# Performance work log

Hardware: AMD Instinct MI355X
Metric: run time of the kernel (lower is better)

Reference implementation:

```python
import jax, jax.numpy as jnp
import numpy as np

DECAY = 0.99
EPS = 1e-5  # Laplace smoothing eps in cluster-size balancing


def _quantize(z_flat, embedding, cluster_size, emb_avg, n_codes):
    # z_flat: [N, D]; embedding: [K, D]
    d = (jnp.sum(z_flat * z_flat, axis=1, keepdims=True)
         + jnp.sum(embedding * embedding, axis=1)
         - 2.0 * (z_flat @ embedding.T))                      # [N, K]
    idx = jnp.argmin(d, axis=1)                               # [N]
    # EMA update (training path). segment_sum == one-hot matmul scatter-add.
    counts = jax.ops.segment_sum(jnp.ones(z_flat.shape[0], z_flat.dtype), idx,
                                 num_segments=n_codes)        # [K]
    new_cs = cluster_size * DECAY + (1.0 - DECAY) * counts
    dw = jax.ops.segment_sum(z_flat, idx, num_segments=n_codes)  # [K, D]
    new_avg = emb_avg * DECAY + (1.0 - DECAY) * dw
    n = new_cs.sum()
    bal = (new_cs + EPS) / (n + n_codes * EPS) * n
    # torch assigns via .data (no autograd) -> stop_gradient for faithfulness
    new_emb = jax.lax.stop_gradient(new_avg / bal[:, None])
    z_q = jnp.take(new_emb, idx, axis=0)  # == one_hot(idx) @ new_emb
    return idx, z_q


def _l2norm(x):
    # F.normalize(x, dim=-1) with eps=1e-12
    return x / jnp.maximum(jnp.linalg.norm(x, axis=-1, keepdims=True), 1e-12)


def reference(z, structure_embedding, style_embedding,
              structure_cluster_size, style_cluster_size,
              structure_embedding_avg, style_embedding_avg):
    b, c, h, w, d = z.shape
    zp = jnp.transpose(z, (0, 2, 3, 4, 1))      # b h w d c
    z_flat = zp.reshape(-1, c)                  # [N, D]
    s_idx, s_q = _quantize(z_flat, structure_embedding, structure_cluster_size,
                           structure_embedding_avg, structure_embedding.shape[0])
    y_idx, y_q = _quantize(z_flat, style_embedding, style_cluster_size,
                           style_embedding_avg, style_embedding.shape[0])

    def back(q):  # [N, C] -> b c h w d
        return jnp.transpose(q.reshape(b, h, w, d, c), (0, 4, 1, 2, 3))

    s_enc = back(s_q)
    y_enc = back(y_q)
    # NOTE: faithful to source — normalize over LAST axis of (b,c,h,w,d),
    # i.e. the spatial depth axis, exactly as F.normalize(dim=-1) does there.
    dis = jnp.mean(jnp.sum(_l2norm(s_enc) * _l2norm(y_enc), axis=-1) ** 2)
    z_q = (s_enc + y_enc) * 0.5
    return z_q, dis, s_idx, y_idx


def setup_inputs() -> dict:
    key = jax.random.key(0)
    k1, k2, k3 = jax.random.split(key, 3)
    B, C, H, W, D = 16, 256, 16, 16, 16
    Ks, Ky = 1024, 512
    return {
        "z": jax.random.normal(k1, (B, C, H, W, D), dtype=jnp.float32),
        "structure_embedding": jax.random.normal(k2, (Ks, C), dtype=jnp.float32),
        "style_embedding": jax.random.normal(k3, (Ky, C), dtype=jnp.float32),
        "structure_cluster_size": jnp.zeros((Ks,), jnp.float32),
        "style_cluster_size": jnp.zeros((Ky,), jnp.float32),
        "structure_embedding_avg": jnp.zeros((Ks, C), jnp.float32),
        "style_embedding_avg": jnp.zeros((Ky, C), jnp.float32),
    }
```

## Files before the change

kernel.cpp:

```cpp
#include <hip/hip_runtime.h>
#include <float.h>

#define NROWS 65536
#define CDIM  256
#define KS    1024
#define KY    512
#define KTOT  1536
#define SPB   4096

#define WB_CNT_S       0
#define WB_CNT_Y       4096
#define WB_RESCUE_CNT  6144
#define WB_DISACC      6152
#define WB_DW_S        6400
#define WB_DW_Y        1054976
#define WB_ZERO_BYTES  1579264
#define WB_EIMG        1579264
#define WB_EN2         2365696
#define WB_IDXS_I      2371840
#define WB_IDXY_I      2633984
#define WB_RLIST_S     2896128
#define WB_RLIST_Y     3158272
#define WB_BASE_S      3420416
#define WB_BASE_Y      3424512
#define WB_CUR_S       3426560
#define WB_CUR_Y       3430656
#define WB_SCALE_S     3432704
#define WB_SCALE_Y     3436800
#define WB_PERM_S      3438848
#define WB_PERM_Y      3700992
#define WB_KSORT_S     3963136
#define WB_KSORT_Y     4225280
#define WB_EMB_S       4487424
#define WB_EMB_Y       5536000

#define OFF_OUT_ZQ   0
#define OFF_OUT_DIS  16777216
#define OFF_OUT_SIDX 16777217
#define OFF_OUT_YIDX 16842753

typedef __attribute__((ext_vector_type(8)))  _Float16 f16x8;
typedef __attribute__((ext_vector_type(4)))  float    f32x4;

__device__ __forceinline__ unsigned int umn(unsigned int a, unsigned int b) { return a < b ? a : b; }
__device__ __forceinline__ unsigned int umx(unsigned int a, unsigned int b) { return a > b ? a : b; }

__global__ void prep_e(const float* __restrict__ Es, const float* __restrict__ Ey,
                       unsigned short* __restrict__ eimg, float* __restrict__ en2) {
    int k = blockIdx.x;
    int lane = threadIdx.x;
    const float* E = (k < KS) ? (Es + (size_t)k * CDIM) : (Ey + (size_t)(k - KS) * CDIM);
    float4 v = *(const float4*)(E + lane * 4);
    float nrm = v.x * v.x + v.y * v.y + v.z * v.z + v.w * v.w;
#pragma unroll
    for (int off = 32; off > 0; off >>= 1) nrm += __shfl_down(nrm, off);
    if (lane == 0) en2[k] = nrm;

    unsigned short q0 = __builtin_bit_cast(unsigned short, (_Float16)v.x);
    unsigned short q1 = __builtin_bit_cast(unsigned short, (_Float16)v.y);
    unsigned short q2 = __builtin_bit_cast(unsigned short, (_Float16)v.z);
    unsigned short q3 = __builtin_bit_cast(unsigned short, (_Float16)v.w);
    uint2 hp = make_uint2((unsigned)q0 | ((unsigned)q1 << 16),
                          (unsigned)q2 | ((unsigned)q3 << 16));

    int c0 = lane * 4;
    int kc = c0 >> 5, g = (c0 >> 3) & 3, j0 = c0 & 7;
    size_t byteoff = (size_t)(k >> 4) * 8192 + (size_t)kc * 1024
                   + (size_t)(g * 16 + (k & 15)) * 16 + (size_t)j0 * 2;
    *(uint2*)((char*)eimg + byteoff) = hp;
}

__global__ void prep_z(const float* __restrict__ z, float* __restrict__ zf) {
    __shared__ float Zs[32][257];
    int blk = blockIdx.x;
    int n0 = blk * 32, b = n0 >> 12, s0 = n0 & 4095;
    int t = threadIdx.x;
    const float* zb = z + (size_t)b * CDIM * SPB + s0;
#pragma unroll
    for (int i = 0; i < 32; ++i) {
        int l = i * 256 + t;
        int c = l >> 5, s = l & 31;
        Zs[s][c] = zb[(size_t)c * SPB + s];
    }
    __syncthreads();
#pragma unroll
    for (int j = 0; j < 8; ++j) {
        int gid = j * 256 + t;
        int nl = gid >> 6, fg = gid & 63;
        float4 v = *(const float4*)(&Zs[nl][fg * 4]);
        *(float4*)(&zf[(size_t)(n0 + nl) * 256 + fg * 4]) = v;
    }
}

__device__ __forceinline__ void stage_phase(const unsigned short* __restrict__ eimg,
                                            int phase, char* lds, int wave, int lane) {
    const char* gs = (const char*)eimg + (size_t)phase * 16384 + wave * 4096 + lane * 16;
    char* ls = lds + wave * 4096;
#pragma unroll
    for (int i = 0; i < 4; ++i)
        __builtin_amdgcn_global_load_lds(
            (const __attribute__((address_space(1))) void*)(gs + i * 1024),
            (__attribute__((address_space(3))) void*)(ls + i * 1024), 16, 0, 0);
}

#define WAITV(n)                                                               \
    asm volatile("s_waitcnt vmcnt(" #n ")");                                   \
    __builtin_amdgcn_sched_barrier(0);

#define FLUSH(book, fo, io, cb, rl)                                            \
    {                                                                          \
        _Pragma("unroll")                                                      \
        for (int rg = 0; rg < 2; ++rg)                                         \
        _Pragma("unroll")                                                      \
        for (int q = 0; q < 4; ++q) {                                          \
            unsigned int v1 = m1a[rg][q], v2 = m2a[rg][q];                     \
            _Pragma("unroll")                                                  \
            for (int m = 8; m >= 1; m >>= 1) {                                 \
                unsigned int o1 = (unsigned int)__shfl_xor((int)v1, m);        \
                unsigned int o2 = (unsigned int)__shfl_xor((int)v2, m);        \
                v2 = umn(umn(v2, o2), umx(v1, o1));                            \
                v1 = umn(v1, o1);                                              \
            }                                                                  \
            if ((lane & 15) == 0) {                                            \
                int kw = (int)(v1 & 0x7FFu) - ((book) ? KS : 0);               \
                int n = n0 + rg * 16 + (lane >> 4) * 4 + q;                    \
                fo[n] = (float)kw;                                             \
                io[n] = kw;                                                    \
                atomicAdd(&cb[kw], 1);                                         \
                if ((v1 >> 11) + 4 > (v2 >> 11)) {                             \
                    int k2w = (int)(v2 & 0x7FFu) - ((book) ? KS : 0);          \
                    int pp = atomicAdd(&rescue_cnt[book], 1);                  \
                    if (pp < 65536) rl[pp] = n | (k2w << 16);                  \
                }                                                              \
            }                                                                  \
            m1a[rg][q] = 0xFFFFFFFFu; m2a[rg][q] = 0xFFFFFFFFu;                \
        }                                                                      \
    }

__launch_bounds__(256, 2)
__global__ void assign_kernel(const float* __restrict__ zf, const unsigned short* __restrict__ eimg,
                              const float* __restrict__ en2,
                              float* __restrict__ sidx_f, float* __restrict__ yidx_f,
                              int* __restrict__ sidx_i, int* __restrict__ yidx_i,
                              int* __restrict__ cnt_s, int* __restrict__ cnt_y,
                              int* __restrict__ rescue_cnt,
                              int* __restrict__ rlist_s, int* __restrict__ rlist_y) {
    __shared__ char sh[4][16384];
    const int tid = threadIdx.x, wave = tid >> 6, lane = tid & 63;
    const int n0 = blockIdx.x * 128 + wave * 32;

    f16x8 A[2][8];
#pragma unroll
    for (int rg = 0; rg < 2; ++rg) {
        const float* zr = zf + (size_t)(n0 + rg * 16 + (lane & 15)) * 256 + (lane >> 4) * 8;
#pragma unroll
        for (int kc = 0; kc < 8; ++kc) {
            float4 f0 = *(const float4*)(zr + kc * 32);
            float4 f1 = *(const float4*)(zr + kc * 32 + 4);
            f16x8 a;
            a[0] = (_Float16)f0.x; a[1] = (_Float16)f0.y;
            a[2] = (_Float16)f0.z; a[3] = (_Float16)f0.w;
            a[4] = (_Float16)f1.x; a[5] = (_Float16)f1.y;
            a[6] = (_Float16)f1.z; a[7] = (_Float16)f1.w;
            A[rg][kc] = a;
        }
    }

    unsigned int m1a[2][4], m2a[2][4];
#pragma unroll
    for (int rg = 0; rg < 2; ++rg)
#pragma unroll
        for (int q = 0; q < 4; ++q) { m1a[rg][q] = 0xFFFFFFFFu; m2a[rg][q] = 0xFFFFFFFFu; }

    stage_phase(eimg, 0, &sh[0][0], wave, lane);
    stage_phase(eimg, 1, &sh[1][0], wave, lane);

#pragma unroll 1
    for (int p = 0; p < 48; ++p) {
        if (p + 2 < 48) stage_phase(eimg, p + 2, &sh[(p + 2) & 3][0], wave, lane);
        if (p < 46)       { WAITV(8); }
        else if (p == 46) { WAITV(4); }
        else              { WAITV(0); }
        __builtin_amdgcn_s_barrier();
        asm volatile("" ::: "memory");

#pragma unroll
        for (int c = 0; c < 2; ++c) {
            const char* bb = &sh[p & 3][c * 8192] + lane * 16;
            f32x4 acc0 = {}, acc1 = {};
#pragma unroll
            for (int kc = 0; kc < 8; ++kc) {
                f16x8 B = *(const f16x8*)(bb + kc * 1024);
                acc0 = __builtin_amdgcn_mfma_f32_16x16x32_f16(A[0][kc], B, acc0, 0, 0, 0);
                acc1 = __builtin_amdgcn_mfma_f32_16x16x32_f16(A[1][kc], B, acc1, 0, 0, 0);
            }
            const int kcode = (2 * p + c) * 16 + (lane & 15);
            const float en0 = en2[kcode] + 512.0f;
            const unsigned int tag = (unsigned int)kcode;
#pragma unroll
            for (int q = 0; q < 4; ++q) {
                float d0 = fmaf(-2.f, acc0[q], en0);
                unsigned int du0 = (__float_as_uint(d0) & 0xFFFFF800u) | tag;
                m2a[0][q] = umn(m2a[0][q], umx(m1a[0][q], du0));
                m1a[0][q] = umn(m1a[0][q], du0);
                float d1 = fmaf(-2.f, acc1[q], en0);
                unsigned int du1 = (__float_as_uint(d1) & 0xFFFFF800u) | tag;
                m2a[1][q] = umn(m2a[1][q], umx(m1a[1][q], du1));
                m1a[1][q] = umn(m1a[1][q], du1);
            }
        }
        asm volatile("" ::: "memory");

        if (p == 31) FLUSH(0, sidx_f, sidx_i, cnt_s, rlist_s);
    }
    FLUSH(1, yidx_f, yidx_i, cnt_y, rlist_y);
}

__global__ void rescue2_kernel(const float* __restrict__ zf,
                               const float* __restrict__ Es, const float* __restrict__ Ey,
                               const float* __restrict__ en2, const int* __restrict__ rcnt,
                               const int* __restrict__ rlist_s, const int* __restrict__ rlist_y,
                               float* __restrict__ sidx_f, float* __restrict__ yidx_f,
                               int* __restrict__ sidx_i, int* __restrict__ yidx_i,
                               int* __restrict__ cnt_s, int* __restrict__ cnt_y) {
    int cs = rcnt[0]; if (cs > 65536) cs = 65536;
    int cy = rcnt[1]; if (cy > 65536) cy = 65536;
    int total = cs + cy;
    const int lane = threadIdx.x & 63;
    const int nw = (gridDim.x * blockDim.x) >> 6;
    for (int e = (int)((blockIdx.x * blockDim.x + threadIdx.x) >> 6); e < total; e += nw) {
        int book = (e >= cs);
        unsigned int ent = (unsigned int)(book ? rlist_y[e - cs] : rlist_s[e]);
        int n  = (int)(ent & 0xFFFFu);
        int k2 = (int)(ent >> 16);
        int* idx_i = book ? yidx_i : sidx_i;
        float* idx_f = book ? yidx_f : sidx_f;
        int* cnt = book ? cnt_y : cnt_s;
        const float* E = book ? Ey : Es;
        const float* en2k = book ? (en2 + KS) : en2;
        int k1 = idx_i[n];
        float4 zv = *(const float4*)(zf + (size_t)n * 256 + lane * 4);
        float4 a  = *(const float4*)(E + (size_t)k1 * 256 + lane * 4);
        float4 c  = *(const float4*)(E + (size_t)k2 * 256 + lane * 4);
        float d1 = zv.x * a.x + zv.y * a.y + zv.z * a.z + zv.w * a.w;
        float d2 = zv.x * c.x + zv.y * c.y + zv.z * c.z + zv.w * c.w;
#pragma unroll
        for (int off = 32; off > 0; off >>= 1) {
            d1 += __shfl_down(d1, off);
            d2 += __shfl_down(d2, off);
        }
        if (lane == 0) {
            float dist1 = en2k[k1] - 2.f * d1;
            float dist2 = en2k[k2] - 2.f * d2;
            int nk = (dist2 < dist1 || (dist2 == dist1 && k2 < k1)) ? k2 : k1;
            if (nk != k1) {
                atomicSub(&cnt[k1], 1);
                atomicAdd(&cnt[nk], 1);
                idx_i[n] = nk;
                idx_f[n] = (float)nk;
            }
        }
    }
}

__global__ void scanbal_kernel(const float* __restrict__ cs_in, const float* __restrict__ cy_in,
                               const int* __restrict__ cnt_s, const int* __restrict__ cnt_y,
                               int* __restrict__ base_s, int* __restrict__ base_y,
                               int* __restrict__ cur_s, int* __restrict__ cur_y,
                               float* __restrict__ scale_s, float* __restrict__ scale_y) {
    __shared__ int   sc[1024];
    __shared__ float sf[1024];
    int K = blockIdx.x ? KY : KS;
    const float* csi = blockIdx.x ? cy_in : cs_in;
    const int*   cnt = blockIdx.x ? cnt_y : cnt_s;
    int* base = blockIdx.x ? base_y : base_s;
    int* cur  = blockIdx.x ? cur_y  : cur_s;
    float* scale = blockIdx.x ? scale_y : scale_s;
    int t = threadIdx.x;
    int c = (t < K) ? cnt[t] : 0;
    float ncs = (t < K) ? (csi[t] * 0.99f + 0.01f * (float)c) : 0.f;
    sc[t] = c;
    __syncthreads();
    for (int off = 1; off < 1024; off <<= 1) {
        int v = sc[t] + ((t >= off) ? sc[t - off] : 0);
        __syncthreads();
        sc[t] = v;
        __syncthreads();
    }
    int incl = sc[t];
    sf[t] = ncs;
    __syncthreads();
    for (int s2 = 512; s2 > 0; s2 >>= 1) {
        if (t < s2) sf[t] += sf[t + s2];
        __syncthreads();
    }
    float nsum = sf[0];
    if (t < K) {
        base[t] = incl - c;
        cur[t]  = incl - c;
        float bal = (ncs + 1e-5f) / (nsum + (float)K * 1e-5f) * nsum;
        scale[t] = 1.0f / bal;
    }
}

__global__ void scatter_kernel(const int* __restrict__ si, const int* __restrict__ yi,
                               int* __restrict__ cur_s, int* __restrict__ cur_y,
                               int* __restrict__ perm_s, int* __restrict__ perm_y,
                               int* __restrict__ ksort_s, int* __restrict__ ksort_y) {
    int i = blockIdx.x * 256 + threadIdx.x;
    if (i < NROWS) {
        int k = si[i]; int p = atomicAdd(&cur_s[k], 1);
        perm_s[p] = i; ksort_s[p] = k;
    } else {
        int n = i - NROWS; int k = yi[n]; int p = atomicAdd(&cur_y[k], 1);
        perm_y[p] = n; ksort_y[p] = k;
    }
}

__global__ void dw_kernel(const float* __restrict__ zf,
                          const int* __restrict__ perm_s, const int* __restrict__ ksort_s,
                          const int* __restrict__ perm_y, const int* __restrict__ ksort_y,
                          float* __restrict__ dw_s, float* __restrict__ dw_y) {
    __shared__ int keys[33];
    __shared__ int rows[32];
    const int t = threadIdx.x;
    int blk = blockIdx.x;
    const int* perm; const int* ks; float* dw; int p0;
    if (blk < NROWS / 32) { perm = perm_s; ks = ksort_s; dw = dw_s; p0 = blk * 32; }
    else                  { perm = perm_y; ks = ksort_y; dw = dw_y; p0 = (blk - NROWS / 32) * 32; }
    if (t < 32) { keys[t] = ks[p0 + t]; rows[t] = perm[p0 + t]; }
    if (t == 32) keys[32] = -1;
    __syncthreads();
    float acc = 0.f;
#pragma unroll 8
    for (int j = 0; j < 32; ++j) {
        acc += zf[(size_t)rows[j] * 256 + t];
        if (keys[j + 1] != keys[j]) {
            atomicAdd(&dw[(size_t)keys[j] * 256 + t], acc);
            acc = 0.f;
        }
    }
}

__global__ void embnew_kernel(const float* __restrict__ avg_s, const float* __restrict__ avg_y,
                              const float* __restrict__ dw_s, const float* __restrict__ dw_y,
                              const float* __restrict__ scale_s, const float* __restrict__ scale_y,
                              float* __restrict__ emb_s, float* __restrict__ emb_y) {
    int id = blockIdx.x, t = threadIdx.x;
    if (id < KS) { int i = id * 256 + t; emb_s[i] = (avg_s[i] * 0.99f + 0.01f * dw_s[i]) * scale_s[id]; }
    else { int kk = id - KS; int i = kk * 256 + t; emb_y[i] = (avg_y[i] * 0.99f + 0.01f * dw_y[i]) * scale_y[kk]; }
}

__global__ void gather_kernel(const float* __restrict__ Se, const float* __restrict__ Ye,
                              const int* __restrict__ sidx, const int* __restrict__ yidx,
                              float* __restrict__ zq, float* __restrict__ disacc) {
    __shared__ float qb[256 * 17];
    __shared__ int   si[16], yi[16];
    __shared__ float red[256];
    const int g  = blockIdx.x;
    const int b  = g >> 8;
    const int hw = g & 255;
    const int t  = threadIdx.x;
    if (t < 16) {
        int n = b * SPB + hw * 16 + t;
        si[t] = sidx[n];
        yi[t] = yidx[n];
    }
    __syncthreads();
    float ns = 0.f, ny = 0.f, dot = 0.f;
#pragma unroll
    for (int d = 0; d < 16; ++d) {
        float s = Se[(size_t)si[d] * CDIM + t];
        float y = Ye[(size_t)yi[d] * CDIM + t];
        ns  = fmaf(s, s, ns);
        ny  = fmaf(y, y, ny);
        dot = fmaf(s, y, dot);
        qb[t * 17 + d] = 0.5f * (s + y);
    }
    float den = fmaxf(sqrtf(ns), 1e-12f) * fmaxf(sqrtf(ny), 1e-12f);
    float val = dot / den;
    red[t] = val * val;
    __syncthreads();
    for (int s = 128; s > 0; s >>= 1) {
        if (t < s) red[t] += red[t + s];
        __syncthreads();
    }
    if (t == 0) atomicAdd(disacc, red[0]);
    float* zg = zq + (size_t)b * CDIM * SPB + hw * 16;
#pragma unroll
    for (int j = 0; j < 16; ++j) {
        int e = j * 256 + t;
        int c = e >> 4, d = e & 15;
        zg[(size_t)c * SPB + d] = qb[c * 17 + d];
    }
}

__global__ void fin_kernel(const float* __restrict__ disacc, float* __restrict__ out_dis) {
    *out_dis = *disacc * (1.0f / 1048576.0f);
}

extern "C" void kernel_launch(void* const* d_in, const int* in_sizes, int n_in,
                              void* d_out, int out_size, void* d_ws, size_t ws_size,
                              hipStream_t stream) {
    const float* z     = (const float*)d_in[0];
    const float* Es    = (const float*)d_in[1];
    const float* Ey    = (const float*)d_in[2];
    const float* s_cs  = (const float*)d_in[3];
    const float* y_cs  = (const float*)d_in[4];
    const float* s_avg = (const float*)d_in[5];
    const float* y_avg = (const float*)d_in[6];
    float* out = (float*)d_out;
    char*  w   = (char*)d_ws;

    unsigned short* eimg = (unsigned short*)(w + WB_EIMG);
    float* en2    = (float*)(w + WB_EN2);
    int* idxs_i   = (int*)(w + WB_IDXS_I);
    int* idxy_i   = (int*)(w + WB_IDXY_I);
    int* cnt_s    = (int*)(w + WB_CNT_S);
    int* cnt_y    = (int*)(w + WB_CNT_Y);
    int* r_cnt    = (int*)(w + WB_RESCUE_CNT);
    int* rlist_s  = (int*)(w + WB_RLIST_S);
    int* rlist_y  = (int*)(w + WB_RLIST_Y);
    int* base_s   = (int*)(w + WB_BASE_S);
    int* base_y   = (int*)(w + WB_BASE_Y);
    int* cur_s    = (int*)(w + WB_CUR_S);
    int* cur_y    = (int*)(w + WB_CUR_Y);
    float* scale_s = (float*)(w + WB_SCALE_S);
    float* scale_y = (float*)(w + WB_SCALE_Y);
    int* perm_s   = (int*)(w + WB_PERM_S);
    int* perm_y   = (int*)(w + WB_PERM_Y);
    int* ksort_s  = (int*)(w + WB_KSORT_S);
    int* ksort_y  = (int*)(w + WB_KSORT_Y);
    float* dw_s   = (float*)(w + WB_DW_S);
    float* dw_y   = (float*)(w + WB_DW_Y);
    float* emb_s  = (float*)(w + WB_EMB_S);
    float* emb_y  = (float*)(w + WB_EMB_Y);

    float* zf     = out + OFF_OUT_ZQ;
    float* sidx_f = out + OFF_OUT_SIDX;
    float* yidx_f = out + OFF_OUT_YIDX;

    hipMemsetAsync(w, 0, WB_ZERO_BYTES, stream);

    prep_e<<<KTOT, 64, 0, stream>>>(Es, Ey, eimg, en2);
    prep_z<<<NROWS / 32, 256, 0, stream>>>(z, zf);

    assign_kernel<<<NROWS / 128, 256, 0, stream>>>(zf, eimg, en2, sidx_f, yidx_f,
                                                   idxs_i, idxy_i, cnt_s, cnt_y,
                                                   r_cnt, rlist_s, rlist_y);

    rescue2_kernel<<<512, 256, 0, stream>>>(zf, Es, Ey, en2, r_cnt, rlist_s, rlist_y,
                                            sidx_f, yidx_f, idxs_i, idxy_i, cnt_s, cnt_y);

    scanbal_kernel<<<2, 1024, 0, stream>>>(s_cs, y_cs, cnt_s, cnt_y, base_s, base_y,
                                           cur_s, cur_y, scale_s, scale_y);
    scatter_kernel<<<2 * NROWS / 256, 256, 0, stream>>>(idxs_i, idxy_i, cur_s, cur_y,
                                                        perm_s, perm_y, ksort_s, ksort_y);
    dw_kernel<<<2 * NROWS / 32, 256, 0, stream>>>(zf, perm_s, ksort_s, perm_y, ksort_y, dw_s, dw_y);
    embnew_kernel<<<KTOT, 256, 0, stream>>>(s_avg, y_avg, dw_s, dw_y, scale_s, scale_y, emb_s, emb_y);
    gather_kernel<<<4096, 256, 0, stream>>>(emb_s, emb_y, idxs_i, idxy_i,
                                            out + OFF_OUT_ZQ, (float*)(w + WB_DISACC));
    fin_kernel<<<1, 1, 0, stream>>>((float*)(w + WB_DISACC), out + OFF_OUT_DIS);
}
```

Before: 321.9 us.

## Split codebook scan across two blocks per row tile with partial-min merge kernel

The assignment kernel now launches two blocks per 128-row tile. Each block scans half of the 1536 combined codes (48 chunks of 16), and the structure book's halves are joined in a new merge kernel that combines per-row top-2 partial results. Staging is reworked to 8 KB chunks with a 3-deep prefetch, code norms are cached in LDS, and launch bounds rise to 4 blocks per CU for more occupancy. In exchange it adds a kernel launch, writes and rereads the partial top-2 buffers, and loads the A fragments twice per row tile.

```diff
diff --git a/kernel.cpp b/kernel.cpp
--- a/kernel.cpp
+++ b/kernel.cpp
@@ -92,22 +92,23 @@
     }
 }
 
-__device__ __forceinline__ void stage_phase(const unsigned short* __restrict__ eimg,
-                                            int phase, char* lds, int wave, int lane) {
-    const char* gs = (const char*)eimg + (size_t)phase * 16384 + wave * 4096 + lane * 16;
-    char* ls = lds + wave * 4096;
-#pragma unroll
-    for (int i = 0; i < 4; ++i)
-        __builtin_amdgcn_global_load_lds(
-            (const __attribute__((address_space(1))) void*)(gs + i * 1024),
-            (__attribute__((address_space(3))) void*)(ls + i * 1024), 16, 0, 0);
+__device__ __forceinline__ void stage1(const unsigned short* __restrict__ eimg,
+                                       int chunk, char* lds, int wave, int lane) {
+    const char* gs = (const char*)eimg + (size_t)chunk * 8192 + wave * 2048 + lane * 16;
+    char* ls = lds + wave * 2048;
+    __builtin_amdgcn_global_load_lds(
+        (const __attribute__((address_space(1))) void*)gs,
+        (__attribute__((address_space(3))) void*)ls, 16, 0, 0);
+    __builtin_amdgcn_global_load_lds(
+        (const __attribute__((address_space(1))) void*)(gs + 1024),
+        (__attribute__((address_space(3))) void*)(ls + 1024), 16, 0, 0);
 }
 
 #define WAITV(n)                                                               \
     asm volatile("s_waitcnt vmcnt(" #n ")");                                   \
     __builtin_amdgcn_sched_barrier(0);
 
-#define FLUSH(book, fo, io, cb, rl)                                            \
+#define PSFLUSH(dst)                                                           \
     {                                                                          \
         _Pragma("unroll")                                                      \
         for (int rg = 0; rg < 2; ++rg)                                         \
@@ -122,32 +123,57 @@
                 v1 = umn(v1, o1);                                              \
             }                                                                  \
             if ((lane & 15) == 0) {                                            \
-                int kw = (int)(v1 & 0x7FFu) - ((book) ? KS : 0);               \
                 int n = n0 + rg * 16 + (lane >> 4) * 4 + q;                    \
-                fo[n] = (float)kw;                                             \
-                io[n] = kw;                                                    \
-                atomicAdd(&cb[kw], 1);                                         \
-                if ((v1 >> 11) + 4 > (v2 >> 11)) {                             \
-                    int k2w = (int)(v2 & 0x7FFu) - ((book) ? KS : 0);          \
-                    int pp = atomicAdd(&rescue_cnt[book], 1);                  \
-                    if (pp < 65536) rl[pp] = n | (k2w << 16);                  \
-                }                                                              \
+                dst[n] = make_uint2(v1, v2);                                   \
             }                                                                  \
             m1a[rg][q] = 0xFFFFFFFFu; m2a[rg][q] = 0xFFFFFFFFu;                \
         }                                                                      \
     }
 
-__launch_bounds__(256, 2)
+#define FLUSHY()                                                               \
+    {                                                                          \
+        _Pragma("unroll")                                                      \
+        for (int rg = 0; rg < 2; ++rg)                                         \
+        _Pragma("unroll")                                                      \
+        for (int q = 0; q < 4; ++q) {                                          \
+            unsigned int v1 = m1a[rg][q], v2 = m2a[rg][q];                     \
+            _Pragma("unroll")                                                  \
+            for (int m = 8; m >= 1; m >>= 1) {                                 \
+                unsigned int o1 = (unsigned int)__shfl_xor((int)v1, m);        \
+                unsigned int o2 = (unsigned int)__shfl_xor((int)v2, m);        \
+                v2 = umn(umn(v2, o2), umx(v1, o1));                            \
+                v1 = umn(v1, o1);                                              \
+            }                                                                  \
+            if ((lane & 15) == 0) {                                            \
+                int kw = (int)(v1 & 0x7FFu) - KS;                              \
+                int n = n0 + rg * 16 + (lane >> 4) * 4 + q;                    \
+                yidx_f[n] = (float)kw;                                         \
+                yidx_i[n] = kw;                                                \
+                atomicAdd(&cnt_y[kw], 1);                                      \
+                if ((v1 >> 11) + 4 > (v2 >> 11)) {                             \
+                    int k2w = (int)(v2 & 0x7FFu) - KS;                         \
+                    int pp = atomicAdd(&rescue_cnt[1], 1);                     \
+                    if (pp < 65536) rlist_y[pp] = n | (k2w << 16);             \
+                }                                                              \
+            }                                                                  \
+        }                                                                      \
+    }
+
+__launch_bounds__(256, 4)
 __global__ void assign_kernel(const float* __restrict__ zf, const unsigned short* __restrict__ eimg,
-                              const float* __restrict__ en2,
-                              float* __restrict__ sidx_f, float* __restrict__ yidx_f,
-                              int* __restrict__ sidx_i, int* __restrict__ yidx_i,
-                              int* __restrict__ cnt_s, int* __restrict__ cnt_y,
-                              int* __restrict__ rescue_cnt,
-                              int* __restrict__ rlist_s, int* __restrict__ rlist_y) {
-    __shared__ char sh[4][16384];
+                              const float* __restrict__ en2g,
+                              uint2* __restrict__ ps0, uint2* __restrict__ ps1,
+                              float* __restrict__ yidx_f, int* __restrict__ yidx_i,
+                              int* __restrict__ cnt_y, int* __restrict__ rescue_cnt,
+                              int* __restrict__ rlist_y) {
+    __shared__ char  sh[4][8192];
+    __shared__ float en2l[KTOT];
     const int tid = threadIdx.x, wave = tid >> 6, lane = tid & 63;
-    const int n0 = blockIdx.x * 128 + wave * 32;
+    const int half = blockIdx.x & 1;
+    const int n0 = (blockIdx.x >> 1) * 128 + wave * 32;
+    const int cb = half * 48;
+
+    for (int i = tid; i < KTOT; i += 256) en2l[i] = en2g[i];
 
     f16x8 A[2][8];
 #pragma unroll
@@ -172,48 +198,68 @@
 #pragma unroll
         for (int q = 0; q < 4; ++q) { m1a[rg][q] = 0xFFFFFFFFu; m2a[rg][q] = 0xFFFFFFFFu; }
 
-    stage_phase(eimg, 0, &sh[0][0], wave, lane);
-    stage_phase(eimg, 1, &sh[1][0], wave, lane);
+    stage1(eimg, cb + 0, &sh[0][0], wave, lane);
+    stage1(eimg, cb + 1, &sh[1][0], wave, lane);
+    stage1(eimg, cb + 2, &sh[2][0], wave, lane);
+    __syncthreads();
 
 #pragma unroll 1
-    for (int p = 0; p < 48; ++p) {
-        if (p + 2 < 48) stage_phase(eimg, p + 2, &sh[(p + 2) & 3][0], wave, lane);
-        if (p < 46)       { WAITV(8); }
-        else if (p == 46) { WAITV(4); }
+    for (int i = 0; i < 48; ++i) {
+        if (i < 46)       { WAITV(4); }
+        else if (i == 46) { WAITV(2); }
         else              { WAITV(0); }
         __builtin_amdgcn_s_barrier();
         asm volatile("" ::: "memory");
-
-#pragma unroll
-        for (int c = 0; c < 2; ++c) {
-            const char* bb = &sh[p & 3][c * 8192] + lane * 16;
-            f32x4 acc0 = {}, acc1 = {};
-#pragma unroll
-            for (int kc = 0; kc < 8; ++kc) {
-                f16x8 B = *(const f16x8*)(bb + kc * 1024);
-                acc0 = __builtin_amdgcn_mfma_f32_16x16x32_f16(A[0][kc], B, acc0, 0, 0, 0);
-                acc1 = __builtin_amdgcn_mfma_f32_16x16x32_f16(A[1][kc], B, acc1, 0, 0, 0);
-            }
-            const int kcode = (2 * p + c) * 16 + (lane & 15);
-            const float en0 = en2[kcode] + 512.0f;
-            const unsigned int tag = (unsigned int)kcode;
-#pragma unroll
-            for (int q = 0; q < 4; ++q) {
-                float d0 = fmaf(-2.f, acc0[q], en0);
-                unsigned int du0 = (__float_as_uint(d0) & 0xFFFFF800u) | tag;
-                m2a[0][q] = umn(m2a[0][q], umx(m1a[0][q], du0));
-                m1a[0][q] = umn(m1a[0][q], du0);
-                float d1 = fmaf(-2.f, acc1[q], en0);
-                unsigned int du1 = (__float_as_uint(d1) & 0xFFFFF800u) | tag;
-                m2a[1][q] = umn(m2a[1][q], umx(m1a[1][q], du1));
-                m1a[1][q] = umn(m1a[1][q], du1);
-            }
+        if (i + 3 < 48) stage1(eimg, cb + i + 3, &sh[(i + 3) & 3][0], wave, lane);
+
+        const int chunk = cb + i;
+        const char* bb = &sh[i & 3][0] + lane * 16;
+        f32x4 acc0 = {}, acc1 = {};
+#pragma unroll
+        for (int kc = 0; kc < 8; ++kc) {
+            f16x8 B = *(const f16x8*)(bb + kc * 1024);
+            acc0 = __builtin_amdgcn_mfma_f32_16x16x32_f16(A[0][kc], B, acc0, 0, 0, 0);
+            acc1 = __builtin_amdgcn_mfma_f32_16x16x32_f16(A[1][kc], B, acc1, 0, 0, 0);
         }
-        asm volatile("" ::: "memory");
-
-        if (p == 31) FLUSH(0, sidx_f, sidx_i, cnt_s, rlist_s);
-    }
-    FLUSH(1, yidx_f, yidx_i, cnt_y, rlist_y);
+        const int kcode = chunk * 16 + (lane & 15);
+        const float en0 = en2l[kcode] + 512.0f;
+        const unsigned int tag = (unsigned int)kcode;
+#pragma unroll
+        for (int q = 0; q < 4; ++q) {
+            float d0 = fmaf(-2.f, acc0[q], en0);
+            unsigned int du0 = (__float_as_uint(d0) & 0xFFFFF800u) | tag;
+            m2a[0][q] = umn(m2a[0][q], umx(m1a[0][q], du0));
+            m1a[0][q] = umn(m1a[0][q], du0);
+            float d1 = fmaf(-2.f, acc1[q], en0);
+            unsigned int du1 = (__float_as_uint(d1) & 0xFFFFF800u) | tag;
+            m2a[1][q] = umn(m2a[1][q], umx(m1a[1][q], du1));
+            m1a[1][q] = umn(m1a[1][q], du1);
+        }
+
+        if (half == 1 && i == 15) PSFLUSH(ps1);
+    }
+
+    if (half == 0) { PSFLUSH(ps0); }
+    else           { FLUSHY(); }
+}
+
+__global__ void merge_s_kernel(const uint2* __restrict__ ps0, const uint2* __restrict__ ps1,
+                               float* __restrict__ sidx_f, int* __restrict__ sidx_i,
+                               int* __restrict__ cnt_s, int* __restrict__ rescue_cnt,
+                               int* __restrict__ rlist_s) {
+    int n = blockIdx.x * 256 + threadIdx.x;
+    uint2 a = ps0[n], b = ps1[n];
+    unsigned int v1 = umn(a.x, b.x);
+    unsigned int v2 = umn(umn(a.y, b.y), umx(a.x, b.x));
+    int kw = (int)(v1 & 0x7FFu);
+    sidx_f[n] = (float)kw;
+    sidx_i[n] = kw;
+    atomicAdd(&cnt_s[kw], 1);
+    if ((v1 >> 11) + 4 > (v2 >> 11)) {
+        int k2w = (int)(v2 & 0x7FFu);
+        int pp = atomicAdd(&rescue_cnt[0], 1);
+        if (pp < 65536) rlist_s[pp] = n | (k2w << 16);
+    }
 }
 
 __global__ void rescue2_kernel(const float* __restrict__ zf,
@@ -435,6 +481,8 @@
     float* dw_y   = (float*)(w + WB_DW_Y);
     float* emb_s  = (float*)(w + WB_EMB_S);
     float* emb_y  = (float*)(w + WB_EMB_Y);
+    uint2* ps0 = (uint2*)(w + WB_EMB_S);
+    uint2* ps1 = ps0 + NROWS;
 
     float* zf     = out + OFF_OUT_ZQ;
     float* sidx_f = out + OFF_OUT_SIDX;
@@ -445,9 +493,11 @@
     prep_e<<<KTOT, 64, 0, stream>>>(Es, Ey, eimg, en2);
     prep_z<<<NROWS / 32, 256, 0, stream>>>(z, zf);
 
-    assign_kernel<<<NROWS / 128, 256, 0, stream>>>(zf, eimg, en2, sidx_f, yidx_f,
-                                                   idxs_i, idxy_i, cnt_s, cnt_y,
-                                                   r_cnt, rlist_s, rlist_y);
+    assign_kernel<<<(NROWS / 128) * 2, 256, 0, stream>>>(
+        zf, eimg, en2, ps0, ps1, yidx_f, idxy_i, cnt_y, r_cnt, rlist_y);
+
+    merge_s_kernel<<<NROWS / 256, 256, 0, stream>>>(ps0, ps1, sidx_f, idxs_i,
+                                                    cnt_s, r_cnt, rlist_s);
 
     rescue2_kernel<<<512, 256, 0, stream>>>(zf, Es, Ey, en2, r_cnt, rlist_s, rlist_y,
                                             sidx_f, yidx_f, idxs_i, idxy_i, cnt_s, cnt_y);
```

New measurement: 342.9 us. 6.5% more time.
